# Performance work log

Measured on AMD Instinct MI355X. Metric: run time of the kernel, lower is better.

Reference implementation:

```python
import jax, jax.numpy as jnp
import numpy as np

# pywt Wavelet('db4') filter bank (8 taps)
_DEC_LO = np.array([-0.010597401785069032, 0.032883011666982945, 0.030841381835986965,
                    -0.18703481171888114, -0.02798376941698385, 0.6308807679295904,
                    0.7148465705525415, 0.23037781330885523], dtype=np.float32)
_REC_LO = _DEC_LO[::-1].copy()
_DEC_HI = (np.array([(-1.0) ** (k + 1) for k in range(8)], dtype=np.float32) * _REC_LO)
_REC_HI = _DEC_HI[::-1].copy()
_FLEN = 8
_LEVEL = 3


def _corr(x, filt, stride):
    # x: (N, L); cross-correlation with `filt`, VALID, given stride -> (N, Lout)
    k = jnp.asarray(filt.copy())[None, None, :].astype(x.dtype)
    y = jax.lax.conv_general_dilated(x[:, None, :], k, (stride,), 'VALID',
                                     dimension_numbers=('NCH', 'OIH', 'NCH'))
    return y[:, 0, :]


def _dwt(x):
    # pywt dwt, mode='symmetric': pad F-1 each side, full convolution, keep odd phase
    p = _FLEN - 1
    ext = jnp.pad(x, ((0, 0), (p, p)), mode='symmetric')[:, 1:]
    cA = _corr(ext, _DEC_LO[::-1], 2)  # conv == corr with flipped filter
    cD = _corr(ext, _DEC_HI[::-1], 2)
    return cA, cD


def _idwt(a, d):
    # pywt idwt: upsample by 2 (values at even idx), full conv, trim F-2 each side
    n = a.shape[-1]

    def up(c):
        # upsampled (2n-1) with 1 zero of padding on each side -> length 2n+1
        u = jnp.zeros((c.shape[0], 2 * n + 1), c.dtype)
        return u.at[:, 1::2].set(c)

    return _corr(up(a), _REC_LO[::-1], 1) + _corr(up(d), _REC_HI[::-1], 1)


def _waverec(a, details):
    # details ordered coarsest -> finest (as pywt waverec consumes them)
    for d in details:
        if a.shape[-1] == d.shape[-1] + 1:
            a = a[:, :-1]
        a = _idwt(a, d)
    return a


def setup_inputs() -> dict:
    key = jax.random.key(0)
    x = jax.random.normal(key, (32, 64, 16384), dtype=jnp.float32)
    return {"x": x}


def reference(x):
    B, F, L = x.shape
    x2 = x.reshape(B * F, L)

    # wavedec: repeatedly split the approximation
    a = x2
    details = []  # finest first
    for _ in range(_LEVEL):
        a, d = _dwt(a)
        details.append(d)
    details = details[::-1]  # coarsest -> finest, matching waverec order

    low = _waverec(a, [jnp.zeros_like(d) for d in details])
    high = _waverec(jnp.zeros_like(a), details)

    low = low[:, :L].reshape(B, F, L)
    high = high[:, :L].reshape(B, F, L)
    return (low, high)
```

## Files before the change

### kernel.cpp

```cpp
#include <hip/hip_runtime.h>

namespace {
constexpr int kL0      = 16384;
constexpr int kN1      = 8195;
constexpr int kN2      = 4101;
constexpr int kTS      = 2048;
constexpr int kTilesPerRow = kL0 / kTS;
constexpr int kThreads = 256;

constexpr int SX  = 2138;
constexpr int SA1 = 1066;
constexpr int SA2 = 530;
constexpr int SA3 = 262;

constexpr float RLc[8] = {
     0.23037781330885523f,  0.7148465705525415f,   0.6308807679295904f,
    -0.02798376941698385f, -0.18703481171888114f,  0.030841381835986965f,
     0.032883011666982945f, -0.010597401785069032f };

struct WT { float w[8][7]; };
constexpr WT make_w() {
    WT W{};
    for (int r = 0; r < 8; ++r) {
        const int r2 = r >> 1, pi = r & 1;
        for (int u = 0; u < 4; ++u) {
            const float cu = RLc[6 + pi - 2 * u];
            const int k = r2 + u, k2 = k >> 1, pk = k & 1;
            for (int s = 0; s < 4; ++s) {
                const float cs = RLc[6 + pk - 2 * s];
                const int j = k2 + s, j2 = j >> 1, pj = j & 1;
                for (int t = 0; t < 4; ++t)
                    W.w[r][j2 + t] += cu * cs * RLc[6 + pj - 2 * t];
            }
        }
    }
    return W;
}

__device__ constexpr float RL[8] = {
     0.23037781330885523f,  0.7148465705525415f,   0.6308807679295904f,
    -0.02798376941698385f, -0.18703481171888114f,  0.030841381835986965f,
     0.032883011666982945f, -0.010597401785069032f };
__device__ constexpr WT W = make_w();
}

__device__ __forceinline__ int reflect(int g, int N) {
    if (g < 0)  g = -1 - g;
    if (g >= N) g = 2 * N - 1 - g;
    return g;
}

__device__ __forceinline__ float tap8(const float* __restrict__ p) {
    const float2* q = reinterpret_cast<const float2*>(p);
    const float2 q0 = q[0], q1 = q[1], q2 = q[2], q3 = q[3];
    float s = q0.x * RL[0];
    s = fmaf(q0.y, RL[1], s); s = fmaf(q1.x, RL[2], s); s = fmaf(q1.y, RL[3], s);
    s = fmaf(q2.x, RL[4], s); s = fmaf(q2.y, RL[5], s); s = fmaf(q3.x, RL[6], s);
    s = fmaf(q3.y, RL[7], s);
    return s;
}

__global__ void __launch_bounds__(kThreads, 8)
wavelet_tiled(const float* __restrict__ x, float* __restrict__ out, int rows) {
    __shared__ float sx [SX];
    __shared__ float sa1[SA1];
    __shared__ float sa2[SA2];
    __shared__ float sa3[SA3];

    const int tid  = threadIdx.x;
    const int row  = blockIdx.x / kTilesPerRow;
    const int tile = blockIdx.x % kTilesPerRow;
    const int O  = tile * kTS;
    const int X0 = O - 42;
    const int A0 = (O >> 1) - 18;
    const int B0 = (O >> 2) - 6;
    const float* __restrict__ xr = x + (size_t)row * kL0;

    const int t0  = (tile == 0) ? 42 : 2;
    const int thi = (tile == kTilesPerRow - 1) ? 2090 : SX;
    const int Nv  = (thi - t0) >> 2;
    for (int v = tid; v < Nv; v += kThreads) {
        const float4 val = *reinterpret_cast<const float4*>(xr + X0 + t0 + 4 * v);
        float2* dst = reinterpret_cast<float2*>(&sx[t0 + 4 * v]);
        dst[0] = make_float2(val.x, val.y);
        dst[1] = make_float2(val.z, val.w);
    }
    for (int t = tid; t < SX; t += kThreads)
        if (t < t0 || t >= t0 + 4 * Nv)
            sx[t] = xr[reflect(X0 + t, kL0)];
    __syncthreads();

    for (int m = tid; m < SA1; m += kThreads) {
        const int ng = reflect(A0 + m, kN1);
        sa1[m] = tap8(&sx[2 * (ng - A0)]);
    }
    __syncthreads();

    for (int m = tid; m < SA2; m += kThreads) {
        const int ng = reflect(B0 + m, kN2);
        sa2[m] = tap8(&sa1[2 * (ng - B0)]);
    }
    __syncthreads();

    for (int m = tid; m < SA3; m += kThreads)
        sa3[m] = tap8(&sa2[2 * m]);
    __syncthreads();

    float a[7];
    #pragma unroll
    for (int m = 0; m < 7; ++m) a[m] = sa3[tid + m];

    float lo[8];
    #pragma unroll
    for (int r = 0; r < 8; ++r) {
        float s = a[0] * W.w[r][0];
        #pragma unroll
        for (int m = 1; m < 7; ++m) s = fmaf(a[m], W.w[r][m], s);
        lo[r] = s;
    }

    const float4* xr4 = reinterpret_cast<const float4*>(xr + O + 8 * tid);
    const float4 xv0 = xr4[0], xv1 = xr4[1];
    float* __restrict__ lowp  = out + (size_t)row * kL0 + O + 8 * tid;
    float* __restrict__ highp = lowp + (size_t)rows * kL0;
    reinterpret_cast<float4*>(lowp)[0]  = make_float4(lo[0], lo[1], lo[2], lo[3]);
    reinterpret_cast<float4*>(lowp)[1]  = make_float4(lo[4], lo[5], lo[6], lo[7]);
    reinterpret_cast<float4*>(highp)[0] = make_float4(xv0.x - lo[0], xv0.y - lo[1],
                                                      xv0.z - lo[2], xv0.w - lo[3]);
    reinterpret_cast<float4*>(highp)[1] = make_float4(xv1.x - lo[4], xv1.y - lo[5],
                                                      xv1.z - lo[6], xv1.w - lo[7]);
}

extern "C" void kernel_launch(void* const* d_in, const int* in_sizes, int n_in,
                              void* d_out, int out_size, void* d_ws, size_t ws_size,
                              hipStream_t stream) {
    (void)n_in; (void)d_ws; (void)ws_size; (void)out_size;
    const float* x = (const float*)d_in[0];
    float* out = (float*)d_out;
    const int rows = in_sizes[0] / kL0;
    const int blocks = rows * kTilesPerRow;
    hipLaunchKernelGGL(wavelet_tiled, dim3(blocks), dim3(kThreads), 0, stream,
                       x, out, rows);
}
```

Measured before the change: 101.9 us.

## Shrink tiles to one wavefront each with even/odd split LDS layout

Reduces the tile from 2048 to 512 outputs, giving each wavefront its own tile with a private LDS region, two wavefronts per block. Inputs and intermediate approximations are stored split into even/odd planes to avoid strided LDS access, and each lane computes several consecutive outputs from register-cached windows. This aims to raise occupancy and cut LDS bank conflicts, at the cost of a larger relative halo (more redundant global reads and compute per output).

```diff
diff --git a/kernel.cpp b/kernel.cpp
--- a/kernel.cpp
+++ b/kernel.cpp
@@ -1,17 +1,24 @@
 #include <hip/hip_runtime.h>
 
 namespace {
-constexpr int kL0      = 16384;
-constexpr int kN1      = 8195;
-constexpr int kN2      = 4101;
-constexpr int kTS      = 2048;
+constexpr int kL0 = 16384;
+constexpr int kN1 = 8195;
+constexpr int kN2 = 4101;
+constexpr int kTS = 512;
 constexpr int kTilesPerRow = kL0 / kTS;
-constexpr int kThreads = 256;
-
-constexpr int SX  = 2138;
-constexpr int SA1 = 1066;
-constexpr int SA2 = 530;
-constexpr int SA3 = 262;
+constexpr int kWaves = 2;
+constexpr int kThreads = 64 * kWaves;
+
+constexpr int SX  = 602;
+constexpr int SA1 = 298;
+constexpr int SA2 = 146;
+constexpr int SA3 = 70;
+
+constexpr int XE = 0,   XO = 302;
+constexpr int A1E = 604, A1O = 754;
+constexpr int A2E = 904, A2O = 978;
+constexpr int S3 = 1052;
+constexpr int REG = 1124;
 
 constexpr float RLc[8] = {
      0.23037781330885523f,  0.7148465705525415f,   0.6308807679295904f,
@@ -50,85 +57,135 @@
     return g;
 }
 
-__device__ __forceinline__ float tap8(const float* __restrict__ p) {
-    const float2* q = reinterpret_cast<const float2*>(p);
-    const float2 q0 = q[0], q1 = q[1], q2 = q[2], q3 = q[3];
-    float s = q0.x * RL[0];
-    s = fmaf(q0.y, RL[1], s); s = fmaf(q1.x, RL[2], s); s = fmaf(q1.y, RL[3], s);
-    s = fmaf(q2.x, RL[4], s); s = fmaf(q2.y, RL[5], s); s = fmaf(q3.x, RL[6], s);
-    s = fmaf(q3.y, RL[7], s);
+__device__ __forceinline__ float tap_pp(const float* __restrict__ R,
+                                        int Ebase, int Obase, int mh) {
+    float s = R[Ebase + mh] * RL[0];
+    s = fmaf(R[Obase + mh],     RL[1], s);
+    s = fmaf(R[Ebase + mh + 1], RL[2], s);
+    s = fmaf(R[Obase + mh + 1], RL[3], s);
+    s = fmaf(R[Ebase + mh + 2], RL[4], s);
+    s = fmaf(R[Obase + mh + 2], RL[5], s);
+    s = fmaf(R[Ebase + mh + 3], RL[6], s);
+    s = fmaf(R[Obase + mh + 3], RL[7], s);
     return s;
 }
 
 __global__ void __launch_bounds__(kThreads, 8)
-wavelet_tiled(const float* __restrict__ x, float* __restrict__ out, int rows) {
-    __shared__ float sx [SX];
-    __shared__ float sa1[SA1];
-    __shared__ float sa2[SA2];
-    __shared__ float sa3[SA3];
-
-    const int tid  = threadIdx.x;
-    const int row  = blockIdx.x / kTilesPerRow;
-    const int tile = blockIdx.x % kTilesPerRow;
+wavelet_wave(const float* __restrict__ x, float* __restrict__ out, int rows) {
+    __shared__ float lds[kWaves * REG];
+    const int lane = threadIdx.x & 63;
+    const int wv   = threadIdx.x >> 6;
+    float* __restrict__ R = lds + wv * REG;
+
+    const int row  = blockIdx.x >> 4;
+    const int tile = ((blockIdx.x & 15) << 1) | wv;
     const int O  = tile * kTS;
     const int X0 = O - 42;
     const int A0 = (O >> 1) - 18;
     const int B0 = (O >> 2) - 6;
     const float* __restrict__ xr = x + (size_t)row * kL0;
-
-    const int t0  = (tile == 0) ? 42 : 2;
-    const int thi = (tile == kTilesPerRow - 1) ? 2090 : SX;
-    const int Nv  = (thi - t0) >> 2;
-    for (int v = tid; v < Nv; v += kThreads) {
-        const float4 val = *reinterpret_cast<const float4*>(xr + X0 + t0 + 4 * v);
-        float2* dst = reinterpret_cast<float2*>(&sx[t0 + 4 * v]);
-        dst[0] = make_float2(val.x, val.y);
-        dst[1] = make_float2(val.z, val.w);
-    }
-    for (int t = tid; t < SX; t += kThreads)
-        if (t < t0 || t >= t0 + 4 * Nv)
-            sx[t] = xr[reflect(X0 + t, kL0)];
-    __syncthreads();
-
-    for (int m = tid; m < SA1; m += kThreads) {
-        const int ng = reflect(A0 + m, kN1);
-        sa1[m] = tap8(&sx[2 * (ng - A0)]);
-    }
-    __syncthreads();
-
-    for (int m = tid; m < SA2; m += kThreads) {
-        const int ng = reflect(B0 + m, kN2);
-        sa2[m] = tap8(&sa1[2 * (ng - B0)]);
-    }
-    __syncthreads();
-
-    for (int m = tid; m < SA3; m += kThreads)
-        sa3[m] = tap8(&sa2[2 * m]);
-    __syncthreads();
-
-    float a[7];
-    #pragma unroll
-    for (int m = 0; m < 7; ++m) a[m] = sa3[tid + m];
-
-    float lo[8];
-    #pragma unroll
-    for (int r = 0; r < 8; ++r) {
-        float s = a[0] * W.w[r][0];
+    const bool edge = (tile == 0) || (tile == kTilesPerRow - 1);
+
+    if (!edge) {
+        for (int v = lane; v < 150; v += 64) {
+            const int g = X0 + 4 * v;
+            const float2 f0 = *reinterpret_cast<const float2*>(xr + g);
+            const float2 f1 = *reinterpret_cast<const float2*>(xr + g + 2);
+            *reinterpret_cast<float2*>(&R[XE + 2 * v]) = make_float2(f0.x, f1.x);
+            *reinterpret_cast<float2*>(&R[XO + 2 * v]) = make_float2(f0.y, f1.y);
+        }
+        if (lane == 0) { R[XE + 300] = xr[X0 + 600]; R[XO + 300] = xr[X0 + 601]; }
+    } else {
+        for (int t = lane; t < SX; t += 64) {
+            const float v = xr[reflect(X0 + t, kL0)];
+            R[((t & 1) ? XO : XE) + (t >> 1)] = v;
+        }
+    }
+    __syncthreads();
+
+    {
+        const int m0 = 5 * lane;
+        const int c  = (m0 < SA1) ? ((SA1 - m0 < 5) ? SA1 - m0 : 5) : 0;
+        if (c == 5 && (A0 + m0) >= 0 && (A0 + m0 + 4) < kN1) {
+            float e[8], o[8];
+            #pragma unroll
+            for (int j = 0; j < 8; ++j) { e[j] = R[XE + m0 + j]; o[j] = R[XO + m0 + j]; }
+            #pragma unroll
+            for (int i = 0; i < 5; ++i) {
+                float s = e[i] * RL[0];
+                s = fmaf(o[i],     RL[1], s); s = fmaf(e[i + 1], RL[2], s);
+                s = fmaf(o[i + 1], RL[3], s); s = fmaf(e[i + 2], RL[4], s);
+                s = fmaf(o[i + 2], RL[5], s); s = fmaf(e[i + 3], RL[6], s);
+                s = fmaf(o[i + 3], RL[7], s);
+                const int m = m0 + i;
+                R[((m & 1) ? A1O : A1E) + (m >> 1)] = s;
+            }
+        } else if (c > 0) {
+            for (int i = 0; i < c; ++i) {
+                const int m  = m0 + i;
+                const int mh = reflect(A0 + m, kN1) - A0;
+                const float s = tap_pp(R, XE, XO, mh);
+                R[((m & 1) ? A1O : A1E) + (m >> 1)] = s;
+            }
+        }
+    }
+    __syncthreads();
+
+    {
+        const int m0 = 3 * lane;
+        const int c  = (m0 < SA2) ? ((SA2 - m0 < 3) ? SA2 - m0 : 3) : 0;
+        if (c == 3 && (B0 + m0) >= 0 && (B0 + m0 + 2) < kN2) {
+            float e[6], o[6];
+            #pragma unroll
+            for (int j = 0; j < 6; ++j) { e[j] = R[A1E + m0 + j]; o[j] = R[A1O + m0 + j]; }
+            #pragma unroll
+            for (int i = 0; i < 3; ++i) {
+                float s = e[i] * RL[0];
+                s = fmaf(o[i],     RL[1], s); s = fmaf(e[i + 1], RL[2], s);
+                s = fmaf(o[i + 1], RL[3], s); s = fmaf(e[i + 2], RL[4], s);
+                s = fmaf(o[i + 2], RL[5], s); s = fmaf(e[i + 3], RL[6], s);
+                s = fmaf(o[i + 3], RL[7], s);
+                const int m = m0 + i;
+                R[((m & 1) ? A2O : A2E) + (m >> 1)] = s;
+            }
+        } else if (c > 0) {
+            for (int i = 0; i < c; ++i) {
+                const int m  = m0 + i;
+                const int mh = reflect(B0 + m, kN2) - B0;
+                const float s = tap_pp(R, A1E, A1O, mh);
+                R[((m & 1) ? A2O : A2E) + (m >> 1)] = s;
+            }
+        }
+    }
+    __syncthreads();
+
+    for (int t = lane; t < SA3; t += 64)
+        R[S3 + t] = tap_pp(R, A2E, A2O, t);
+    __syncthreads();
+
+    {
+        float a[7];
         #pragma unroll
-        for (int m = 1; m < 7; ++m) s = fmaf(a[m], W.w[r][m], s);
-        lo[r] = s;
-    }
-
-    const float4* xr4 = reinterpret_cast<const float4*>(xr + O + 8 * tid);
-    const float4 xv0 = xr4[0], xv1 = xr4[1];
-    float* __restrict__ lowp  = out + (size_t)row * kL0 + O + 8 * tid;
-    float* __restrict__ highp = lowp + (size_t)rows * kL0;
-    reinterpret_cast<float4*>(lowp)[0]  = make_float4(lo[0], lo[1], lo[2], lo[3]);
-    reinterpret_cast<float4*>(lowp)[1]  = make_float4(lo[4], lo[5], lo[6], lo[7]);
-    reinterpret_cast<float4*>(highp)[0] = make_float4(xv0.x - lo[0], xv0.y - lo[1],
-                                                      xv0.z - lo[2], xv0.w - lo[3]);
-    reinterpret_cast<float4*>(highp)[1] = make_float4(xv1.x - lo[4], xv1.y - lo[5],
-                                                      xv1.z - lo[6], xv1.w - lo[7]);
+        for (int m = 0; m < 7; ++m) a[m] = R[S3 + lane + m];
+        float lo[8];
+        #pragma unroll
+        for (int r = 0; r < 8; ++r) {
+            float s = a[0] * W.w[r][0];
+            #pragma unroll
+            for (int m = 1; m < 7; ++m) s = fmaf(a[m], W.w[r][m], s);
+            lo[r] = s;
+        }
+        const float4* xr4 = reinterpret_cast<const float4*>(xr + O + 8 * lane);
+        const float4 xv0 = xr4[0], xv1 = xr4[1];
+        float* __restrict__ lowp  = out + (size_t)row * kL0 + O + 8 * lane;
+        float* __restrict__ highp = lowp + (size_t)rows * kL0;
+        reinterpret_cast<float4*>(lowp)[0]  = make_float4(lo[0], lo[1], lo[2], lo[3]);
+        reinterpret_cast<float4*>(lowp)[1]  = make_float4(lo[4], lo[5], lo[6], lo[7]);
+        reinterpret_cast<float4*>(highp)[0] = make_float4(xv0.x - lo[0], xv0.y - lo[1],
+                                                          xv0.z - lo[2], xv0.w - lo[3]);
+        reinterpret_cast<float4*>(highp)[1] = make_float4(xv1.x - lo[4], xv1.y - lo[5],
+                                                          xv1.z - lo[6], xv1.w - lo[7]);
+    }
 }
 
 extern "C" void kernel_launch(void* const* d_in, const int* in_sizes, int n_in,
@@ -138,7 +195,7 @@
     const float* x = (const float*)d_in[0];
     float* out = (float*)d_out;
     const int rows = in_sizes[0] / kL0;
-    const int blocks = rows * kTilesPerRow;
-    hipLaunchKernelGGL(wavelet_tiled, dim3(blocks), dim3(kThreads), 0, stream,
+    const int blocks = rows * (kTilesPerRow / kWaves);
+    hipLaunchKernelGGL(wavelet_wave, dim3(blocks), dim3(kThreads), 0, stream,
                        x, out, rows);
 }
```

Result: slower. 124.1 us (+21.8%).

## Use direct global-to-LDS loads and vectorized 4-output stencil stages

Applied to the files above, without the earlier changes.

Interior tiles now stage input into shared memory with global_load_lds (async direct-to-LDS) instead of register-staged float4 loads, with the tile base shifted for 16-byte alignment. Each decimation level computes four outputs per thread from four float4 LDS reads, cutting LDS instruction count and per-element reflect logic; boundary elements fall back to scalar paths. Moving the x reload before the final compute also hides its latency. This adds alignment-dependent indexing and more boundary-case complexity.

```diff
diff --git a/kernel.cpp b/kernel.cpp
--- a/kernel.cpp
+++ b/kernel.cpp
@@ -1,14 +1,13 @@
 #include <hip/hip_runtime.h>
 
 namespace {
-constexpr int kL0      = 16384;
-constexpr int kN1      = 8195;
-constexpr int kN2      = 4101;
-constexpr int kTS      = 2048;
-constexpr int kTilesPerRow = kL0 / kTS;
+constexpr int kL0 = 16384;
+constexpr int kN1 = 8195;
+constexpr int kN2 = 4101;
+constexpr int kTS = 2048;
 constexpr int kThreads = 256;
 
-constexpr int SX  = 2138;
+constexpr int SXL = 2308;
 constexpr int SA1 = 1066;
 constexpr int SA2 = 530;
 constexpr int SA3 = 262;
@@ -50,85 +49,164 @@
     return g;
 }
 
-__device__ __forceinline__ float tap8(const float* __restrict__ p) {
-    const float2* q = reinterpret_cast<const float2*>(p);
-    const float2 q0 = q[0], q1 = q[1], q2 = q[2], q3 = q[3];
-    float s = q0.x * RL[0];
-    s = fmaf(q0.y, RL[1], s); s = fmaf(q1.x, RL[2], s); s = fmaf(q1.y, RL[3], s);
-    s = fmaf(q2.x, RL[4], s); s = fmaf(q2.y, RL[5], s); s = fmaf(q3.x, RL[6], s);
-    s = fmaf(q3.y, RL[7], s);
+__device__ __forceinline__ float tap8s(const float* __restrict__ p) {
+    float s = p[0] * RL[0];
+    s = fmaf(p[1], RL[1], s); s = fmaf(p[2], RL[2], s);
+    s = fmaf(p[3], RL[3], s); s = fmaf(p[4], RL[4], s);
+    s = fmaf(p[5], RL[5], s); s = fmaf(p[6], RL[6], s);
+    s = fmaf(p[7], RL[7], s);
     return s;
 }
+
+typedef __attribute__((address_space(1))) const void gvoid_t;
+typedef __attribute__((address_space(3))) void lvoid_t;
 
 __global__ void __launch_bounds__(kThreads, 8)
 wavelet_tiled(const float* __restrict__ x, float* __restrict__ out, int rows) {
-    __shared__ float sx [SX];
-    __shared__ float sa1[SA1];
-    __shared__ float sa2[SA2];
-    __shared__ float sa3[SA3];
+    __shared__ __align__(16) float sx [SXL];
+    __shared__ __align__(16) float sa1[1068];
+    __shared__ __align__(16) float sa2[532];
+    __shared__ __align__(16) float sa3[264];
 
     const int tid  = threadIdx.x;
-    const int row  = blockIdx.x / kTilesPerRow;
-    const int tile = blockIdx.x % kTilesPerRow;
-    const int O  = tile * kTS;
-    const int X0 = O - 42;
+    const int row  = blockIdx.x >> 3;
+    const int tile = blockIdx.x & 7;
+    const int O  = tile << 11;
+    const int XB = O - 44;
     const int A0 = (O >> 1) - 18;
     const int B0 = (O >> 2) - 6;
     const float* __restrict__ xr = x + (size_t)row * kL0;
 
-    const int t0  = (tile == 0) ? 42 : 2;
-    const int thi = (tile == kTilesPerRow - 1) ? 2090 : SX;
-    const int Nv  = (thi - t0) >> 2;
-    for (int v = tid; v < Nv; v += kThreads) {
-        const float4 val = *reinterpret_cast<const float4*>(xr + X0 + t0 + 4 * v);
-        float2* dst = reinterpret_cast<float2*>(&sx[t0 + 4 * v]);
-        dst[0] = make_float2(val.x, val.y);
-        dst[1] = make_float2(val.z, val.w);
-    }
-    for (int t = tid; t < SX; t += kThreads)
-        if (t < t0 || t >= t0 + 4 * Nv)
-            sx[t] = xr[reflect(X0 + t, kL0)];
-    __syncthreads();
-
-    for (int m = tid; m < SA1; m += kThreads) {
-        const int ng = reflect(A0 + m, kN1);
-        sa1[m] = tap8(&sx[2 * (ng - A0)]);
-    }
-    __syncthreads();
-
-    for (int m = tid; m < SA2; m += kThreads) {
-        const int ng = reflect(B0 + m, kN2);
-        sa2[m] = tap8(&sa1[2 * (ng - B0)]);
-    }
-    __syncthreads();
-
-    for (int m = tid; m < SA3; m += kThreads)
-        sa3[m] = tap8(&sa2[2 * m]);
-    __syncthreads();
-
-    float a[7];
-    #pragma unroll
-    for (int m = 0; m < 7; ++m) a[m] = sa3[tid + m];
-
-    float lo[8];
-    #pragma unroll
-    for (int r = 0; r < 8; ++r) {
-        float s = a[0] * W.w[r][0];
+    if (tile != 0 && tile != 7) {
+        if (tid < 2) sx[2 + tid] = xr[XB + 2 + tid];
+        const int wv = tid >> 6, lane = tid & 63;
+        for (int c = wv; c < 9; c += 4) {
+            const int fo = 4 + (c << 8) + (lane << 2);
+            __builtin_amdgcn_global_load_lds((gvoid_t*)(xr + XB + fo),
+                                             (lvoid_t*)(&sx[fo]), 16, 0, 0);
+        }
+    } else {
+        const int t0  = (tile == 0) ? 44 : 4;
+        const int thi = (tile == 0) ? 2140 : 2092;
+        const int Nv  = (thi - t0) >> 2;
+        for (int v = tid; v < Nv; v += kThreads) {
+            const float4 val = *reinterpret_cast<const float4*>(xr + XB + t0 + 4 * v);
+            float2* dst = reinterpret_cast<float2*>(&sx[t0 + 4 * v]);
+            dst[0] = make_float2(val.x, val.y);
+            dst[1] = make_float2(val.z, val.w);
+        }
+        for (int t = 2 + tid; t < 2140; t += kThreads)
+            if (t < t0 || t >= thi)
+                sx[t] = xr[reflect(XB + t, kL0)];
+    }
+    __syncthreads();
+
+    for (int p = tid; p < 267; p += kThreads) {
+        const int m0 = 4 * p;
+        if (p < 266 && (A0 + m0) >= 0 && (A0 + m0 + 3) < kN1) {
+            const float4 v0 = *reinterpret_cast<const float4*>(&sx[8 * p]);
+            const float4 v1 = *reinterpret_cast<const float4*>(&sx[8 * p + 4]);
+            const float4 v2 = *reinterpret_cast<const float4*>(&sx[8 * p + 8]);
+            const float4 v3 = *reinterpret_cast<const float4*>(&sx[8 * p + 12]);
+            const float e[16] = {v0.x, v0.y, v0.z, v0.w, v1.x, v1.y, v1.z, v1.w,
+                                 v2.x, v2.y, v2.z, v2.w, v3.x, v3.y, v3.z, v3.w};
+            float o[4];
+            #pragma unroll
+            for (int i = 0; i < 4; ++i) {
+                float s = e[2 + 2 * i] * RL[0];
+                #pragma unroll
+                for (int k = 1; k < 8; ++k) s = fmaf(e[2 + 2 * i + k], RL[k], s);
+                o[i] = s;
+            }
+            *reinterpret_cast<float4*>(&sa1[m0]) = make_float4(o[0], o[1], o[2], o[3]);
+        } else {
+            const int c = (SA1 - m0 < 4) ? (SA1 - m0) : 4;
+            for (int i = 0; i < c; ++i) {
+                const int m  = m0 + i;
+                const int mh = reflect(A0 + m, kN1) - A0;
+                sa1[m] = tap8s(&sx[2 * mh + 2]);
+            }
+        }
+    }
+    __syncthreads();
+
+    if (tid < 133) {
+        const int p = tid, m0 = 4 * p;
+        if (p < 132 && (B0 + m0) >= 0 && (B0 + m0 + 3) < kN2) {
+            const float4 v0 = *reinterpret_cast<const float4*>(&sa1[8 * p]);
+            const float4 v1 = *reinterpret_cast<const float4*>(&sa1[8 * p + 4]);
+            const float4 v2 = *reinterpret_cast<const float4*>(&sa1[8 * p + 8]);
+            const float4 v3 = *reinterpret_cast<const float4*>(&sa1[8 * p + 12]);
+            const float e[16] = {v0.x, v0.y, v0.z, v0.w, v1.x, v1.y, v1.z, v1.w,
+                                 v2.x, v2.y, v2.z, v2.w, v3.x, v3.y, v3.z, v3.w};
+            float o[4];
+            #pragma unroll
+            for (int i = 0; i < 4; ++i) {
+                float s = e[2 * i] * RL[0];
+                #pragma unroll
+                for (int k = 1; k < 8; ++k) s = fmaf(e[2 * i + k], RL[k], s);
+                o[i] = s;
+            }
+            *reinterpret_cast<float4*>(&sa2[m0]) = make_float4(o[0], o[1], o[2], o[3]);
+        } else {
+            const int c = (SA2 - m0 < 4) ? (SA2 - m0) : 4;
+            for (int i = 0; i < c; ++i) {
+                const int m  = m0 + i;
+                const int mh = reflect(B0 + m, kN2) - B0;
+                sa2[m] = tap8s(&sa1[2 * mh]);
+            }
+        }
+    }
+    __syncthreads();
+
+    if (tid < 66) {
+        const int p = tid, m0 = 4 * p;
+        if (p < 65) {
+            const float4 v0 = *reinterpret_cast<const float4*>(&sa2[8 * p]);
+            const float4 v1 = *reinterpret_cast<const float4*>(&sa2[8 * p + 4]);
+            const float4 v2 = *reinterpret_cast<const float4*>(&sa2[8 * p + 8]);
+            const float4 v3 = *reinterpret_cast<const float4*>(&sa2[8 * p + 12]);
+            const float e[16] = {v0.x, v0.y, v0.z, v0.w, v1.x, v1.y, v1.z, v1.w,
+                                 v2.x, v2.y, v2.z, v2.w, v3.x, v3.y, v3.z, v3.w};
+            float o[4];
+            #pragma unroll
+            for (int i = 0; i < 4; ++i) {
+                float s = e[2 * i] * RL[0];
+                #pragma unroll
+                for (int k = 1; k < 8; ++k) s = fmaf(e[2 * i + k], RL[k], s);
+                o[i] = s;
+            }
+            *reinterpret_cast<float4*>(&sa3[m0]) = make_float4(o[0], o[1], o[2], o[3]);
+        } else {
+            sa3[260] = tap8s(&sa2[520]);
+            sa3[261] = tap8s(&sa2[522]);
+        }
+    }
+    __syncthreads();
+
+    {
+        const float4* xr4 = reinterpret_cast<const float4*>(xr + O + 8 * tid);
+        const float4 xv0 = xr4[0], xv1 = xr4[1];
+        float a[7];
         #pragma unroll
-        for (int m = 1; m < 7; ++m) s = fmaf(a[m], W.w[r][m], s);
-        lo[r] = s;
-    }
-
-    const float4* xr4 = reinterpret_cast<const float4*>(xr + O + 8 * tid);
-    const float4 xv0 = xr4[0], xv1 = xr4[1];
-    float* __restrict__ lowp  = out + (size_t)row * kL0 + O + 8 * tid;
-    float* __restrict__ highp = lowp + (size_t)rows * kL0;
-    reinterpret_cast<float4*>(lowp)[0]  = make_float4(lo[0], lo[1], lo[2], lo[3]);
-    reinterpret_cast<float4*>(lowp)[1]  = make_float4(lo[4], lo[5], lo[6], lo[7]);
-    reinterpret_cast<float4*>(highp)[0] = make_float4(xv0.x - lo[0], xv0.y - lo[1],
-                                                      xv0.z - lo[2], xv0.w - lo[3]);
-    reinterpret_cast<float4*>(highp)[1] = make_float4(xv1.x - lo[4], xv1.y - lo[5],
-                                                      xv1.z - lo[6], xv1.w - lo[7]);
+        for (int m = 0; m < 7; ++m) a[m] = sa3[tid + m];
+        float lo[8];
+        #pragma unroll
+        for (int r = 0; r < 8; ++r) {
+            float s = a[0] * W.w[r][0];
+            #pragma unroll
+            for (int m = 1; m < 7; ++m) s = fmaf(a[m], W.w[r][m], s);
+            lo[r] = s;
+        }
+        float* __restrict__ lowp  = out + (size_t)row * kL0 + O + 8 * tid;
+        float* __restrict__ highp = lowp + (size_t)rows * kL0;
+        reinterpret_cast<float4*>(lowp)[0]  = make_float4(lo[0], lo[1], lo[2], lo[3]);
+        reinterpret_cast<float4*>(lowp)[1]  = make_float4(lo[4], lo[5], lo[6], lo[7]);
+        reinterpret_cast<float4*>(highp)[0] = make_float4(xv0.x - lo[0], xv0.y - lo[1],
+                                                          xv0.z - lo[2], xv0.w - lo[3]);
+        reinterpret_cast<float4*>(highp)[1] = make_float4(xv1.x - lo[4], xv1.y - lo[5],
+                                                          xv1.z - lo[6], xv1.w - lo[7]);
+    }
 }
 
 extern "C" void kernel_launch(void* const* d_in, const int* in_sizes, int n_in,
@@ -138,7 +216,7 @@
     const float* x = (const float*)d_in[0];
     float* out = (float*)d_out;
     const int rows = in_sizes[0] / kL0;
-    const int blocks = rows * kTilesPerRow;
+    const int blocks = rows * 8;
     hipLaunchKernelGGL(wavelet_tiled, dim3(blocks), dim3(kThreads), 0, stream,
                        x, out, rows);
 }
```

New measurement: 107.3 us. +5.3%, slower.

## Collapse three decimation levels into one 50-tap stride-8 filter per thread

Applied to the files above, without the earlier changes.

Replaces the shared-memory staged three-level analysis with a single composed 50-tap filter (H3) applied directly from global memory at stride 8, so each thread computes 14 coarse coefficients in registers with no block-wide barriers in interior rows. Boundary coefficients near the row ends are computed separately through small shared buffers using the reflect rules. Blocks become single 64-thread wavefronts covering a quarter row each. In exchange, every thread rereads overlapping input windows from global/L2, does far more FMAs per output, and uses many more registers, and each row is served by far fewer threads.

```diff
diff --git a/kernel.cpp b/kernel.cpp
--- a/kernel.cpp
+++ b/kernel.cpp
@@ -1,17 +1,9 @@
 #include <hip/hip_runtime.h>
 
 namespace {
-constexpr int kL0      = 16384;
-constexpr int kN1      = 8195;
-constexpr int kN2      = 4101;
-constexpr int kTS      = 2048;
-constexpr int kTilesPerRow = kL0 / kTS;
-constexpr int kThreads = 256;
-
-constexpr int SX  = 2138;
-constexpr int SA1 = 1066;
-constexpr int SA2 = 530;
-constexpr int SA3 = 262;
+constexpr int kL0 = 16384;
+constexpr int kN1 = 8195;
+constexpr int kN2 = 4101;
 
 constexpr float RLc[8] = {
      0.23037781330885523f,  0.7148465705525415f,   0.6308807679295904f,
@@ -37,11 +29,22 @@
     return W;
 }
 
+struct H3T { float v[50]; };
+constexpr H3T make_h3() {
+    H3T h{};
+    for (int a = 0; a < 8; ++a)
+        for (int b = 0; b < 8; ++b)
+            for (int c = 0; c < 8; ++c)
+                h.v[4 * a + 2 * b + c] += RLc[a] * RLc[b] * RLc[c];
+    return h;
+}
+
 __device__ constexpr float RL[8] = {
      0.23037781330885523f,  0.7148465705525415f,   0.6308807679295904f,
     -0.02798376941698385f, -0.18703481171888114f,  0.030841381835986965f,
      0.032883011666982945f, -0.010597401785069032f };
 __device__ constexpr WT W = make_w();
+__device__ constexpr H3T H3 = make_h3();
 }
 
 __device__ __forceinline__ int reflect(int g, int N) {
@@ -50,85 +53,112 @@
     return g;
 }
 
-__device__ __forceinline__ float tap8(const float* __restrict__ p) {
-    const float2* q = reinterpret_cast<const float2*>(p);
-    const float2 q0 = q[0], q1 = q[1], q2 = q[2], q3 = q[3];
-    float s = q0.x * RL[0];
-    s = fmaf(q0.y, RL[1], s); s = fmaf(q1.x, RL[2], s); s = fmaf(q1.y, RL[3], s);
-    s = fmaf(q2.x, RL[4], s); s = fmaf(q2.y, RL[5], s); s = fmaf(q3.x, RL[6], s);
-    s = fmaf(q3.y, RL[7], s);
-    return s;
-}
-
-__global__ void __launch_bounds__(kThreads, 8)
-wavelet_tiled(const float* __restrict__ x, float* __restrict__ out, int rows) {
-    __shared__ float sx [SX];
-    __shared__ float sa1[SA1];
-    __shared__ float sa2[SA2];
-    __shared__ float sa3[SA3];
-
-    const int tid  = threadIdx.x;
-    const int row  = blockIdx.x / kTilesPerRow;
-    const int tile = blockIdx.x % kTilesPerRow;
-    const int O  = tile * kTS;
-    const int X0 = O - 42;
-    const int A0 = (O >> 1) - 18;
-    const int B0 = (O >> 2) - 6;
+__global__ void __launch_bounds__(64, 6)
+wavelet_stream(const float* __restrict__ x, float* __restrict__ out, int rows) {
+    const int lane    = threadIdx.x;
+    const int b       = blockIdx.x;
+    const int row     = b >> 2;
+    const int quarter = b & 3;
+    const int t       = (quarter << 6) | lane;
+    const int q0      = t << 3;
     const float* __restrict__ xr = x + (size_t)row * kL0;
 
-    const int t0  = (tile == 0) ? 42 : 2;
-    const int thi = (tile == kTilesPerRow - 1) ? 2090 : SX;
-    const int Nv  = (thi - t0) >> 2;
-    for (int v = tid; v < Nv; v += kThreads) {
-        const float4 val = *reinterpret_cast<const float4*>(xr + X0 + t0 + 4 * v);
-        float2* dst = reinterpret_cast<float2*>(&sx[t0 + 4 * v]);
-        dst[0] = make_float2(val.x, val.y);
-        dst[1] = make_float2(val.z, val.w);
-    }
-    for (int t = tid; t < SX; t += kThreads)
-        if (t < t0 || t >= t0 + 4 * Nv)
-            sx[t] = xr[reflect(X0 + t, kL0)];
-    __syncthreads();
-
-    for (int m = tid; m < SA1; m += kThreads) {
-        const int ng = reflect(A0 + m, kN1);
-        sa1[m] = tap8(&sx[2 * (ng - A0)]);
-    }
-    __syncthreads();
-
-    for (int m = tid; m < SA2; m += kThreads) {
-        const int ng = reflect(B0 + m, kN2);
-        sa2[m] = tap8(&sa1[2 * (ng - B0)]);
-    }
-    __syncthreads();
-
-    for (int m = tid; m < SA3; m += kThreads)
-        sa3[m] = tap8(&sa2[2 * m]);
-    __syncthreads();
-
-    float a[7];
-    #pragma unroll
-    for (int m = 0; m < 7; ++m) a[m] = sa3[tid + m];
-
-    float lo[8];
-    #pragma unroll
-    for (int r = 0; r < 8; ++r) {
-        float s = a[0] * W.w[r][0];
-        #pragma unroll
-        for (int m = 1; m < 7; ++m) s = fmaf(a[m], W.w[r][m], s);
-        lo[r] = s;
+    __shared__ float sa1b[45], sa2b[23], sa3b[12];
+    if (quarter == 0 || quarter == 3) {
+        if (lane < 45) {
+            const int i = (lane < 24) ? lane : 8174 + (lane - 24);
+            float s = 0.f;
+            #pragma unroll
+            for (int k = 0; k < 8; ++k)
+                s = fmaf(xr[reflect(2 * i - 6 + k, kL0)], RL[k], s);
+            sa1b[lane] = s;
+        }
+        __syncthreads();
+        if (lane < 23) {
+            const int j = (lane < 12) ? lane : 4090 + (lane - 12);
+            float s = 0.f;
+            #pragma unroll
+            for (int k = 0; k < 8; ++k) {
+                const int i  = reflect(2 * j - 6 + k, kN1);
+                const int sl = (i <= 23) ? i : 24 + (i - 8174);
+                s = fmaf(sa1b[sl], RL[k], s);
+            }
+            sa2b[lane] = s;
+        }
+        __syncthreads();
+        if (lane < 12) {
+            const int n = (lane < 6) ? lane : 2048 + (lane - 6);
+            float s = 0.f;
+            #pragma unroll
+            for (int k = 0; k < 8; ++k) {
+                const int j  = reflect(2 * n - 6 + k, kN2);
+                const int sl = (j <= 11) ? j : 12 + (j - 4090);
+                s = fmaf(sa2b[sl], RL[k], s);
+            }
+            sa3b[lane] = s;
+        }
+        __syncthreads();
     }
 
-    const float4* xr4 = reinterpret_cast<const float4*>(xr + O + 8 * tid);
-    const float4 xv0 = xr4[0], xv1 = xr4[1];
-    float* __restrict__ lowp  = out + (size_t)row * kL0 + O + 8 * tid;
-    float* __restrict__ highp = lowp + (size_t)rows * kL0;
-    reinterpret_cast<float4*>(lowp)[0]  = make_float4(lo[0], lo[1], lo[2], lo[3]);
-    reinterpret_cast<float4*>(lowp)[1]  = make_float4(lo[4], lo[5], lo[6], lo[7]);
-    reinterpret_cast<float4*>(highp)[0] = make_float4(xv0.x - lo[0], xv0.y - lo[1],
-                                                      xv0.z - lo[2], xv0.w - lo[3]);
-    reinterpret_cast<float4*>(highp)[1] = make_float4(xv1.x - lo[4], xv1.y - lo[5],
-                                                      xv1.z - lo[6], xv1.w - lo[7]);
+    float acc[14];
+    if (t >= 1 && t <= 254) {
+        #pragma unroll
+        for (int m = 0; m < 14; ++m) acc[m] = 0.f;
+        const float4* __restrict__ xw4 =
+            reinterpret_cast<const float4*>(xr + (8 * q0 - 48));
+        #pragma unroll
+        for (int c = 0; c < 40; ++c) {
+            const float4 v = xw4[c];
+            #pragma unroll
+            for (int k = 0; k < 4; ++k) {
+                const int e = 4 * c + k;
+                const float vk = (k == 0) ? v.x : (k == 1) ? v.y : (k == 2) ? v.z : v.w;
+                const int mlo = (e >= 55) ? ((e - 48) >> 3) : 0;
+                int mhi = (e >= 6) ? ((e - 6) >> 3) : -1;
+                if (mhi > 13) mhi = 13;
+                #pragma unroll
+                for (int m = mlo; m <= mhi; ++m)
+                    acc[m] = fmaf(vk, H3.v[e - 8 * m - 6], acc[m]);
+            }
+        }
+    } else {
+        #pragma unroll
+        for (int m = 0; m < 14; ++m) {
+            const int n = q0 + m;
+            if (n >= 6 && n <= 2047) {
+                const float* p = xr + (8 * n - 42);
+                float s = 0.f;
+                #pragma unroll
+                for (int j = 0; j < 50; ++j) s = fmaf(p[j], H3.v[j], s);
+                acc[m] = s;
+            } else {
+                acc[m] = sa3b[(n <= 5) ? n : 6 + (n - 2048)];
+            }
+        }
+    }
+
+    float* __restrict__ lowp  = out + (size_t)row * kL0;
+    float* __restrict__ highp = out + (size_t)rows * kL0 + (size_t)row * kL0;
+    #pragma unroll
+    for (int g = 0; g < 8; ++g) {
+        float lo[8];
+        #pragma unroll
+        for (int r = 0; r < 8; ++r) {
+            float s = acc[g] * W.w[r][0];
+            #pragma unroll
+            for (int m = 1; m < 7; ++m) s = fmaf(acc[g + m], W.w[r][m], s);
+            lo[r] = s;
+        }
+        const int o = (q0 + g) << 3;
+        const float4 xv0 = *reinterpret_cast<const float4*>(xr + o);
+        const float4 xv1 = *reinterpret_cast<const float4*>(xr + o + 4);
+        *reinterpret_cast<float4*>(lowp + o)      = make_float4(lo[0], lo[1], lo[2], lo[3]);
+        *reinterpret_cast<float4*>(lowp + o + 4)  = make_float4(lo[4], lo[5], lo[6], lo[7]);
+        *reinterpret_cast<float4*>(highp + o)     = make_float4(xv0.x - lo[0], xv0.y - lo[1],
+                                                                xv0.z - lo[2], xv0.w - lo[3]);
+        *reinterpret_cast<float4*>(highp + o + 4) = make_float4(xv1.x - lo[4], xv1.y - lo[5],
+                                                                xv1.z - lo[6], xv1.w - lo[7]);
+    }
 }
 
 extern "C" void kernel_launch(void* const* d_in, const int* in_sizes, int n_in,
@@ -138,7 +168,7 @@
     const float* x = (const float*)d_in[0];
     float* out = (float*)d_out;
     const int rows = in_sizes[0] / kL0;
-    const int blocks = rows * kTilesPerRow;
-    hipLaunchKernelGGL(wavelet_tiled, dim3(blocks), dim3(kThreads), 0, stream,
+    const int blocks = rows * 4;
+    hipLaunchKernelGGL(wavelet_stream, dim3(blocks), dim3(64), 0, stream,
                        x, out, rows);
 }
```

Measured after the change: 220.7 us. +116.6%, slower.
